# Kernel tuning notes

Hardware: AMD Instinct MI355X
Metric: run time of the kernel (lower is better)

Reference implementation:

```python
import jax, jax.numpy as jnp
import numpy as np

NEG_SLOPE = 0.2  # PyG GATConv default negative_slope


def _edges(B, C):
    # Fully-connected (no self) edges among the FIRST C nodes only (as in original
    # code, which ignores batch when building edge_index), plus self loops on all
    # B*C nodes (PyG GATConv add_self_loops=True default).
    N = B * C
    ij = np.array([(i, j) for i in range(C) for j in range(C) if i != j], dtype=np.int32)
    loops = np.arange(N, dtype=np.int32)
    src = jnp.concatenate([jnp.asarray(ij[:, 0]), jnp.asarray(loops)])
    dst = jnp.concatenate([jnp.asarray(ij[:, 1]), jnp.asarray(loops)])
    return src, dst, N


def _gat_conv(x2d, W, att_src, att_dst, bias, src, dst, N):
    h = x2d @ W                              # [N, Fout] linear projection (no bias)
    a_src = h @ att_src                      # [N] per-node src attention logit
    a_dst = h @ att_dst                      # [N] per-node dst attention logit
    e = jax.nn.leaky_relu(a_src[src] + a_dst[dst], NEG_SLOPE)   # [E] edge scores
    m = jax.ops.segment_max(e, dst, num_segments=N)             # segment softmax
    ex = jnp.exp(e - m[dst])
    denom = jax.ops.segment_sum(ex, dst, num_segments=N)
    alpha = ex / denom[dst]                                     # [E]
    out = jax.ops.segment_sum(alpha[:, None] * h[src], dst, num_segments=N)
    return out + bias


def setup_inputs() -> dict:
    key = jax.random.key(0)
    k1, k2, k3, k4 = jax.random.split(key, 4)
    B, C, Fin, Fout = 2048, 63, 250, 250
    x = jax.random.normal(k1, (B, 1, C, Fin), dtype=jnp.float32)
    W = jax.random.normal(k2, (Fin, Fout), dtype=jnp.float32) / np.sqrt(Fin).astype(np.float32)
    att_src = jax.random.normal(k3, (Fout,), dtype=jnp.float32) / np.sqrt(Fout).astype(np.float32)
    att_dst = jax.random.normal(k4, (Fout,), dtype=jnp.float32) / np.sqrt(Fout).astype(np.float32)
    bias = jnp.zeros((Fout,), dtype=jnp.float32)
    return {"x": x, "W": W, "att_src": att_src, "att_dst": att_dst, "bias": bias}


def reference(x, W, att_src, att_dst, bias):
    B, _, C, F = x.shape
    src, dst, N = _edges(B, C)
    out = _gat_conv(x.reshape(N, F), W, att_src, att_dst, bias, src, dst, N)
    return out.reshape(B, 1, C, -1)   # [B, 1, C, Fout]
```

## Files before the change

### kernel.cpp

```cpp
#include <hip/hip_runtime.h>
#include <hip/hip_bf16.h>

#define FIN 250
#define NROWS 129024
#define NT 8
#define NBLK 1008

typedef short short8 __attribute__((ext_vector_type(8)));
typedef float f32x4 __attribute__((ext_vector_type(4)));

__device__ __forceinline__ short f2bf(float f) {
    __bf16 b = (__bf16)f;
    return __builtin_bit_cast(short, b);
}

#define WAITV(n) asm volatile("s_waitcnt vmcnt(" #n ")" ::: "memory")
#define WAITL    asm volatile("s_waitcnt lgkmcnt(0)" ::: "memory")
#define SCHEDF   __builtin_amdgcn_sched_barrier(0)
#define HWBAR do { asm volatile("" ::: "memory"); __builtin_amdgcn_s_barrier(); \
                   asm volatile("" ::: "memory"); } while (0)

#define AFR0 0
#define AFR1 8192
#define OB   16384

__device__ __forceinline__ void load_tile(uint4 (&lb)[4], const float* __restrict__ x,
                                          const float* __restrict__ xlast,
                                          int tile, int wv, int lane) {
    #pragma unroll
    for (int rr = 0; rr < 4; ++rr) {
        int grow = tile * 16 + wv * 4 + rr;
        const char* g = (grow == NROWS - 1) ? (const char*)xlast
                                            : (const char*)x + (size_t)grow * 1000u;
        lb[rr] = *(const uint4*)(g + lane * 16);
    }
}

__global__ void __launch_bounds__(256)
wt_prep(const float* __restrict__ W, const float* __restrict__ x,
        unsigned* __restrict__ Wt, float* __restrict__ xlast) {
    int i = blockIdx.x * 256 + threadIdx.x;
    unsigned c  = (unsigned)i >> 7;
    unsigned kp = (unsigned)i & 127u;
    unsigned k0 = 2u * kp;
    unsigned lo = 0u, hi = 0u;
    if (c < FIN) {
        if (k0 < FIN)      lo = (unsigned)(unsigned short)f2bf(W[k0 * FIN + c]);
        if (k0 + 1u < FIN) hi = (unsigned)(unsigned short)f2bf(W[(k0 + 1u) * FIN + c]);
    }
    Wt[(c << 7) + kp] = lo | (hi << 16);
    if (blockIdx.x == 0) {
        int t = threadIdx.x;
        xlast[t] = (t < FIN) ? x[(size_t)(NROWS - 1) * FIN + t] : 0.f;
    }
}

__global__ void __launch_bounds__(256, 1)
gat_gemm(const float* __restrict__ x, const unsigned short* __restrict__ Wt,
         const float* __restrict__ xlast, const float* __restrict__ bias,
         float* __restrict__ out)
{
    __shared__ __align__(16) char lds[32768];

    const int tid  = threadIdx.x;
    const int lane = tid & 63;
    const int wv   = tid >> 6;
    const int m    = lane & 15;
    const int kg   = lane >> 4;

    short8 b[4][8];
    #pragma unroll
    for (int f = 0; f < 4; ++f)
        #pragma unroll
        for (int kk = 0; kk < 8; ++kk)
            b[f][kk] = *(const short8*)((const char*)Wt
                         + ((size_t)(wv * 64 + f * 16 + m) << 9) + kk * 64 + kg * 16);

    float bc[4];
    #pragma unroll
    for (int f = 0; f < 4; ++f) {
        int c = wv * 64 + f * 16 + m;
        bc[f] = (c < FIN) ? bias[c] : 0.f;
    }

    char* const ob = lds + OB;
    const int wkk   = lane >> 3;
    const int wkg   = (lane >> 1) & 3;
    const int whalf = lane & 1;
    const unsigned wroff = (unsigned)(wkk * 1024 + wkg * 256 + whalf * 8);

    WAITV(0); SCHEDF;

    const int bid = blockIdx.x;
    uint4 lbA[4], lbB[4];
    load_tile(lbA, x, xlast, bid,        wv, lane);
    load_tile(lbB, x, xlast, bid + NBLK, wv, lane);
    SCHEDF;

    #pragma unroll 1
    for (int i = 0; i < NT; ++i) {
        const int t = bid + i * NBLK;
        switch (i) {
            case 0:      WAITV(4);  break;
            case 1:      WAITV(12); break;
            case NT - 1: WAITV(16); break;
            default:     WAITV(20); break;
        }
        SCHEDF;

        {
            char* const afrD = lds + ((i & 1) ? AFR1 : AFR0);
            const uint4* lb = (i & 1) ? lbB : lbA;
            #pragma unroll
            for (int rr = 0; rr < 4; ++rr) {
                int row = wv * 4 + rr;
                float v0 = __builtin_bit_cast(float, lb[rr].x);
                float v1 = __builtin_bit_cast(float, lb[rr].y);
                float v2 = __builtin_bit_cast(float, lb[rr].z);
                float v3 = __builtin_bit_cast(float, lb[rr].w);
                unsigned lo = (unsigned)(unsigned short)f2bf(v0)
                            | ((unsigned)(unsigned short)f2bf(v1) << 16);
                unsigned hi = (unsigned)(unsigned short)f2bf(v2)
                            | ((unsigned)(unsigned short)f2bf(v3) << 16);
                *(uint2*)(afrD + wroff + (unsigned)(((row ^ wkk) * 16)))
                    = make_uint2(lo, hi);
            }
        }
        SCHEDF;
        if (i + 2 < NT) {
            if (i & 1) load_tile(lbB, x, xlast, t + 2 * NBLK, wv, lane);
            else       load_tile(lbA, x, xlast, t + 2 * NBLK, wv, lane);
        }
        SCHEDF;
        WAITL;
        HWBAR;

        const char* afrD = lds + ((i & 1) ? AFR1 : AFR0);
        f32x4 acc[4];
        #pragma unroll
        for (int f = 0; f < 4; ++f) acc[f] = (f32x4){bc[f], bc[f], bc[f], bc[f]};
        #pragma unroll
        for (int kk = 0; kk < 8; ++kk) {
            short8 af = *(const short8*)(afrD + kk * 1024 + kg * 256 + ((m ^ kk) * 16));
            #pragma unroll
            for (int f = 0; f < 4; ++f)
                acc[f] = __builtin_amdgcn_mfma_f32_16x16x32_bf16(af, b[f][kk], acc[f], 0, 0, 0);
        }

        #pragma unroll
        for (int f = 0; f < 4; ++f)
            #pragma unroll
            for (int j = 0; j < 4; ++j)
                *(float*)(ob + (kg * 4 + j) * 1024 + (unsigned)(wv * 64 + f * 16 + m) * 4)
                    = acc[f][j];
        WAITL;
        HWBAR;

        #pragma unroll
        for (int rr = 0; rr < 4; ++rr) {
            int row = wv * 4 + rr;
            float4 v = *(const float4*)(ob + row * 1024 + lane * 16);
            char* op = (char*)out + ((size_t)t * 16 + row) * 1000u;
            if (lane < 62)  *(float4*)(op + lane * 16) = v;
            if (lane == 62) *(float2*)(op + 992) = make_float2(v.x, v.y);
        }
    }
}

__global__ void __launch_bounds__(1024, 1)
gat_attn(const float* __restrict__ att_src, const float* __restrict__ att_dst,
         float* __restrict__ out)
{
    __shared__ float hs[63 * 252];
    __shared__ float asrc[64], adst[64];
    __shared__ float alpha[63 * 64];

    const int tid = threadIdx.x;

    for (int idx = tid; idx < 63 * FIN; idx += 1024) {
        int r = idx / FIN, f = idx - r * FIN;
        hs[r * 252 + f] = out[idx];
    }
    __syncthreads();

    {
        int r = tid >> 4, t = tid & 15;
        float s1 = 0.f, s2 = 0.f;
        if (r < 63) {
            for (int k = t; k < FIN; k += 16) {
                float h = hs[r * 252 + k];
                s1 += h * att_src[k];
                s2 += h * att_dst[k];
            }
        }
        #pragma unroll
        for (int o = 8; o >= 1; o >>= 1) {
            s1 += __shfl_xor(s1, o, 16);
            s2 += __shfl_xor(s2, o, 16);
        }
        if (r < 63 && t == 0) { asrc[r] = s1; adst[r] = s2; }
    }
    __syncthreads();

    {
        int d = tid >> 4, t = tid & 15;
        if (d < 63) {
            float ad = adst[d];
            float e_[4];
            float mx = -1e30f;
            #pragma unroll
            for (int q = 0; q < 4; ++q) {
                int sdx = t + q * 16;
                float e = -1e30f;
                if (sdx < 63) {
                    e = asrc[sdx] + ad;
                    e = e > 0.f ? e : 0.2f * e;
                }
                e_[q] = e;
                mx = fmaxf(mx, e);
            }
            #pragma unroll
            for (int o = 8; o >= 1; o >>= 1) mx = fmaxf(mx, __shfl_xor(mx, o, 16));
            float den = 0.f;
            #pragma unroll
            for (int q = 0; q < 4; ++q) {
                int sdx = t + q * 16;
                float ex = (sdx < 63) ? __expf(e_[q] - mx) : 0.f;
                e_[q] = ex;
                den += ex;
            }
            #pragma unroll
            for (int o = 8; o >= 1; o >>= 1) den += __shfl_xor(den, o, 16);
            float rd = 1.f / den;
            #pragma unroll
            for (int q = 0; q < 4; ++q) {
                int sdx = t + q * 16;
                if (sdx < 63) alpha[d * 64 + sdx] = e_[q] * rd;
            }
        }
    }
    __syncthreads();

    for (int idx = tid; idx < 63 * FIN; idx += 1024) {
        int d = idx / FIN, f = idx - d * FIN;
        float v = 0.f;
        for (int sdx = 0; sdx < 63; ++sdx)
            v += alpha[d * 64 + sdx] * hs[sdx * 252 + f];
        out[idx] = v;
    }
}

extern "C" void kernel_launch(void* const* d_in, const int* in_sizes, int n_in,
                              void* d_out, int out_size, void* d_ws, size_t ws_size,
                              hipStream_t stream) {
    (void)in_sizes; (void)n_in; (void)ws_size; (void)out_size;
    const float* x        = (const float*)d_in[0];
    const float* W        = (const float*)d_in[1];
    const float* att_src  = (const float*)d_in[2];
    const float* att_dst  = (const float*)d_in[3];
    const float* bias     = (const float*)d_in[4];
    float* out            = (float*)d_out;
    unsigned* Wt          = (unsigned*)d_ws;
    float* xlast          = (float*)((char*)d_ws + 131072);

    wt_prep<<<128, 256, 0, stream>>>(W, x, Wt, xlast);
    gat_gemm<<<NBLK, 256, 0, stream>>>(x, (const unsigned short*)Wt, xlast, bias, out);
    gat_attn<<<1, 1024, 0, stream>>>(att_src, att_dst, out);
}
```

Baseline: 93.50 us.

## Stage swizzled bf16 W in LDS and give each wave whole 16-row tiles

The block now copies the full bf16 W matrix, XOR-swizzled by wt_prep, into 160KB of LDS. Each wave then independently computes full 16x256 output tiles, reading B fragments from LDS instead of holding a 64-column slice in registers. This removes the per-tile block barriers and the LDS staging of outputs, since results go straight to global memory. The grid drops to 252 blocks with one wave per tile, and the next tile's load is overlapped between the two N-halves. The trade-offs are more LDS traffic for B, uncoalesced scalar output stores, and 16 uint4 load registers per lane.

Measured after the change: 106.4 us. 1.14x slower.

```diff
diff --git a/kernel.cpp b/kernel.cpp
--- a/kernel.cpp
+++ b/kernel.cpp
@@ -4,7 +4,8 @@
 #define FIN 250
 #define NROWS 129024
 #define NT 8
-#define NBLK 1008
+#define NBLK 252
+#define NWAVES 1008
 
 typedef short short8 __attribute__((ext_vector_type(8)));
 typedef float f32x4 __attribute__((ext_vector_type(4)));
@@ -17,22 +18,52 @@
 #define WAITV(n) asm volatile("s_waitcnt vmcnt(" #n ")" ::: "memory")
 #define WAITL    asm volatile("s_waitcnt lgkmcnt(0)" ::: "memory")
 #define SCHEDF   __builtin_amdgcn_sched_barrier(0)
-#define HWBAR do { asm volatile("" ::: "memory"); __builtin_amdgcn_s_barrier(); \
-                   asm volatile("" ::: "memory"); } while (0)
-
-#define AFR0 0
-#define AFR1 8192
-#define OB   16384
-
-__device__ __forceinline__ void load_tile(uint4 (&lb)[4], const float* __restrict__ x,
-                                          const float* __restrict__ xlast,
-                                          int tile, int wv, int lane) {
-    #pragma unroll
-    for (int rr = 0; rr < 4; ++rr) {
-        int grow = tile * 16 + wv * 4 + rr;
+
+#define AFR_BASE 131072
+
+__device__ __forceinline__ void load_tile16(uint4 (&lb)[16], const float* __restrict__ x,
+                                            const float* __restrict__ xlast,
+                                            int tile, int lane) {
+    #pragma unroll
+    for (int rr = 0; rr < 16; ++rr) {
+        int grow = tile * 16 + rr;
         const char* g = (grow == NROWS - 1) ? (const char*)xlast
                                             : (const char*)x + (size_t)grow * 1000u;
         lb[rr] = *(const uint4*)(g + lane * 16);
+    }
+}
+
+__device__ __forceinline__ void mfma_half(const char* afr, const char* wt,
+                                          float* __restrict__ out,
+                                          int tile, int half, int m, int kg,
+                                          unsigned bswz, const float (&bcol)[16]) {
+    f32x4 acc[8];
+    #pragma unroll
+    for (int nf = 0; nf < 8; ++nf) {
+        float b = bcol[half * 8 + nf];
+        acc[nf] = (f32x4){b, b, b, b};
+    }
+    const unsigned chbase = (unsigned)(half * 128) * 512u;
+    #pragma unroll
+    for (int kk = 0; kk < 8; ++kk) {
+        short8 af = *(const short8*)(afr + kk * 1024 + kg * 256 + ((m ^ kk) * 16));
+        #pragma unroll
+        for (int nf = 0; nf < 8; ++nf) {
+            unsigned off = chbase + (unsigned)(nf * 16 + m) * 512u
+                         + (((unsigned)(kk * 64 + kg * 16)) ^ bswz);
+            short8 bf = *(const short8*)(wt + off);
+            acc[nf] = __builtin_amdgcn_mfma_f32_16x16x32_bf16(af, bf, acc[nf], 0, 0, 0);
+        }
+    }
+    unsigned obase = ((unsigned)tile * 16 + (unsigned)kg * 4) * FIN
+                   + (unsigned)(half * 128 + m);
+    #pragma unroll
+    for (int nf = 0; nf < 8; ++nf) {
+        if (half == 0 || nf < 7 || m < 10) {
+            #pragma unroll
+            for (int j = 0; j < 4; ++j)
+                out[obase + (unsigned)(j * FIN) + (unsigned)(nf * 16)] = acc[nf][j];
+        }
     }
 }
 
@@ -40,15 +71,16 @@
 wt_prep(const float* __restrict__ W, const float* __restrict__ x,
         unsigned* __restrict__ Wt, float* __restrict__ xlast) {
     int i = blockIdx.x * 256 + threadIdx.x;
-    unsigned c  = (unsigned)i >> 7;
-    unsigned kp = (unsigned)i & 127u;
+    unsigned c  = (unsigned)i & 255u;
+    unsigned kp = (unsigned)i >> 8;
     unsigned k0 = 2u * kp;
     unsigned lo = 0u, hi = 0u;
     if (c < FIN) {
         if (k0 < FIN)      lo = (unsigned)(unsigned short)f2bf(W[k0 * FIN + c]);
         if (k0 + 1u < FIN) hi = (unsigned)(unsigned short)f2bf(W[(k0 + 1u) * FIN + c]);
     }
-    Wt[(c << 7) + kp] = lo | (hi << 16);
+    unsigned off = (c << 9) + ((4u * kp) ^ ((c & 7u) << 4));
+    *(unsigned*)((char*)Wt + off) = lo | (hi << 16);
     if (blockIdx.x == 0) {
         int t = threadIdx.x;
         xlast[t] = (t < FIN) ? x[(size_t)(NROWS - 1) * FIN + t] : 0.f;
@@ -56,11 +88,11 @@
 }
 
 __global__ void __launch_bounds__(256, 1)
-gat_gemm(const float* __restrict__ x, const unsigned short* __restrict__ Wt,
+gat_gemm(const float* __restrict__ x, const unsigned* __restrict__ Wt,
          const float* __restrict__ xlast, const float* __restrict__ bias,
          float* __restrict__ out)
 {
-    __shared__ __align__(16) char lds[32768];
+    __shared__ __align__(16) char lds[163840];
 
     const int tid  = threadIdx.x;
     const int lane = tid & 63;
@@ -68,22 +100,22 @@
     const int m    = lane & 15;
     const int kg   = lane >> 4;
 
-    short8 b[4][8];
-    #pragma unroll
-    for (int f = 0; f < 4; ++f)
-        #pragma unroll
-        for (int kk = 0; kk < 8; ++kk)
-            b[f][kk] = *(const short8*)((const char*)Wt
-                         + ((size_t)(wv * 64 + f * 16 + m) << 9) + kk * 64 + kg * 16);
-
-    float bc[4];
-    #pragma unroll
-    for (int f = 0; f < 4; ++f) {
-        int c = wv * 64 + f * 16 + m;
-        bc[f] = (c < FIN) ? bias[c] : 0.f;
-    }
-
-    char* const ob = lds + OB;
+    {
+        const uint4* s4 = (const uint4*)Wt;
+        uint4* d4 = (uint4*)lds;
+        for (int i = tid; i < 8192; i += 256) d4[i] = s4[i];
+    }
+    __syncthreads();
+
+    const unsigned bswz = ((unsigned)(m & 7)) << 4;
+    float bcol[16];
+    #pragma unroll
+    for (int nf = 0; nf < 16; ++nf) {
+        int c = nf * 16 + m;
+        bcol[nf] = (c < FIN) ? bias[c] : 0.f;
+    }
+
+    char* const afr = lds + AFR_BASE + wv * 8192;
     const int wkk   = lane >> 3;
     const int wkg   = (lane >> 1) & 3;
     const int whalf = lane & 1;
@@ -91,79 +123,36 @@
 
     WAITV(0); SCHEDF;
 
-    const int bid = blockIdx.x;
-    uint4 lbA[4], lbB[4];
-    load_tile(lbA, x, xlast, bid,        wv, lane);
-    load_tile(lbB, x, xlast, bid + NBLK, wv, lane);
-    SCHEDF;
+    const int w0 = blockIdx.x * 4 + wv;
+    uint4 lb[16];
+    load_tile16(lb, x, xlast, w0, lane);
 
     #pragma unroll 1
     for (int i = 0; i < NT; ++i) {
-        const int t = bid + i * NBLK;
-        switch (i) {
-            case 0:      WAITV(4);  break;
-            case 1:      WAITV(12); break;
-            case NT - 1: WAITV(16); break;
-            default:     WAITV(20); break;
-        }
-        SCHEDF;
-
-        {
-            char* const afrD = lds + ((i & 1) ? AFR1 : AFR0);
-            const uint4* lb = (i & 1) ? lbB : lbA;
-            #pragma unroll
-            for (int rr = 0; rr < 4; ++rr) {
-                int row = wv * 4 + rr;
-                float v0 = __builtin_bit_cast(float, lb[rr].x);
-                float v1 = __builtin_bit_cast(float, lb[rr].y);
-                float v2 = __builtin_bit_cast(float, lb[rr].z);
-                float v3 = __builtin_bit_cast(float, lb[rr].w);
-                unsigned lo = (unsigned)(unsigned short)f2bf(v0)
-                            | ((unsigned)(unsigned short)f2bf(v1) << 16);
-                unsigned hi = (unsigned)(unsigned short)f2bf(v2)
-                            | ((unsigned)(unsigned short)f2bf(v3) << 16);
-                *(uint2*)(afrD + wroff + (unsigned)(((row ^ wkk) * 16)))
-                    = make_uint2(lo, hi);
-            }
-        }
-        SCHEDF;
-        if (i + 2 < NT) {
-            if (i & 1) load_tile(lbB, x, xlast, t + 2 * NBLK, wv, lane);
-            else       load_tile(lbA, x, xlast, t + 2 * NBLK, wv, lane);
+        const int t = w0 + i * NWAVES;
+        if (i == 0) { WAITV(0); } else { WAITV(32); }
+        SCHEDF;
+
+        #pragma unroll
+        for (int rr = 0; rr < 16; ++rr) {
+            float v0 = __builtin_bit_cast(float, lb[rr].x);
+            float v1 = __builtin_bit_cast(float, lb[rr].y);
+            float v2 = __builtin_bit_cast(float, lb[rr].z);
+            float v3 = __builtin_bit_cast(float, lb[rr].w);
+            unsigned lo = (unsigned)(unsigned short)f2bf(v0)
+                        | ((unsigned)(unsigned short)f2bf(v1) << 16);
+            unsigned hi = (unsigned)(unsigned short)f2bf(v2)
+                        | ((unsigned)(unsigned short)f2bf(v3) << 16);
+            *(uint2*)(afr + wroff + (unsigned)(((rr ^ wkk) * 16))) = make_uint2(lo, hi);
         }
         SCHEDF;
         WAITL;
-        HWBAR;
-
-        const char* afrD = lds + ((i & 1) ? AFR1 : AFR0);
-        f32x4 acc[4];
-        #pragma unroll
-        for (int f = 0; f < 4; ++f) acc[f] = (f32x4){bc[f], bc[f], bc[f], bc[f]};
-        #pragma unroll
-        for (int kk = 0; kk < 8; ++kk) {
-            short8 af = *(const short8*)(afrD + kk * 1024 + kg * 256 + ((m ^ kk) * 16));
-            #pragma unroll
-            for (int f = 0; f < 4; ++f)
-                acc[f] = __builtin_amdgcn_mfma_f32_16x16x32_bf16(af, b[f][kk], acc[f], 0, 0, 0);
-        }
-
-        #pragma unroll
-        for (int f = 0; f < 4; ++f)
-            #pragma unroll
-            for (int j = 0; j < 4; ++j)
-                *(float*)(ob + (kg * 4 + j) * 1024 + (unsigned)(wv * 64 + f * 16 + m) * 4)
-                    = acc[f][j];
-        WAITL;
-        HWBAR;
-
-        #pragma unroll
-        for (int rr = 0; rr < 4; ++rr) {
-            int row = wv * 4 + rr;
-            float4 v = *(const float4*)(ob + row * 1024 + lane * 16);
-            char* op = (char*)out + ((size_t)t * 16 + row) * 1000u;
-            if (lane < 62)  *(float4*)(op + lane * 16) = v;
-            if (lane == 62) *(float2*)(op + 992) = make_float2(v.x, v.y);
-        }
+        SCHEDF;
+
+        mfma_half(afr, lds, out, t, 0, m, kg, bswz, bcol);
+        if (i + 1 < NT) load_tile16(lb, x, xlast, t + NWAVES, lane);
+        SCHEDF;
+        mfma_half(afr, lds, out, t, 1, m, kg, bswz, bcol);
     }
 }
 
@@ -264,6 +253,6 @@
     float* xlast          = (float*)((char*)d_ws + 131072);
 
     wt_prep<<<128, 256, 0, stream>>>(W, x, Wt, xlast);
-    gat_gemm<<<NBLK, 256, 0, stream>>>(x, (const unsigned short*)Wt, xlast, bias, out);
+    gat_gemm<<<NBLK, 256, 0, stream>>>(x, Wt, xlast, bias, out);
     gat_attn<<<1, 1024, 0, stream>>>(att_src, att_dst, out);
 }
```

## Make each wave load full tile and store output directly, removing block barriers

Applied to the files above, without the earlier changes.

Each wave now loads and converts all 16 input rows into its own private LDS region instead of sharing a block-wide staged tile, so both s_barrier calls disappear. The output is written straight from the MFMA accumulators with strided scalar stores, replacing the LDS staging pass that gave coalesced row writes. Prefetch drops from two tiles ahead to one. In exchange, every wave reads the same input rows, so global and L2 load traffic rises about fourfold, stores become narrow and scattered, and there is less latency hiding in what looks like a bandwidth-bound kernel.

Result: slower. 106.9 us (+14.4%).

```diff
diff --git a/kernel.cpp b/kernel.cpp
--- a/kernel.cpp
+++ b/kernel.cpp
@@ -17,19 +17,13 @@
 #define WAITV(n) asm volatile("s_waitcnt vmcnt(" #n ")" ::: "memory")
 #define WAITL    asm volatile("s_waitcnt lgkmcnt(0)" ::: "memory")
 #define SCHEDF   __builtin_amdgcn_sched_barrier(0)
-#define HWBAR do { asm volatile("" ::: "memory"); __builtin_amdgcn_s_barrier(); \
-                   asm volatile("" ::: "memory"); } while (0)
-
-#define AFR0 0
-#define AFR1 8192
-#define OB   16384
-
-__device__ __forceinline__ void load_tile(uint4 (&lb)[4], const float* __restrict__ x,
-                                          const float* __restrict__ xlast,
-                                          int tile, int wv, int lane) {
+
+__device__ __forceinline__ void load_tile16(uint4 (&lb)[16], const float* __restrict__ x,
+                                            const float* __restrict__ xlast,
+                                            int tile, int lane) {
     #pragma unroll
-    for (int rr = 0; rr < 4; ++rr) {
-        int grow = tile * 16 + wv * 4 + rr;
+    for (int rr = 0; rr < 16; ++rr) {
+        int grow = tile * 16 + rr;
         const char* g = (grow == NROWS - 1) ? (const char*)xlast
                                             : (const char*)x + (size_t)grow * 1000u;
         lb[rr] = *(const uint4*)(g + lane * 16);
@@ -83,7 +77,7 @@
         bc[f] = (c < FIN) ? bias[c] : 0.f;
     }
 
-    char* const ob = lds + OB;
+    char* const afr = lds + wv * 8192;
     const int wkk   = lane >> 3;
     const int wkg   = (lane >> 1) & 3;
     const int whalf = lane & 1;
@@ -92,77 +86,55 @@
     WAITV(0); SCHEDF;
 
     const int bid = blockIdx.x;
-    uint4 lbA[4], lbB[4];
-    load_tile(lbA, x, xlast, bid,        wv, lane);
-    load_tile(lbB, x, xlast, bid + NBLK, wv, lane);
+    uint4 lb[16];
+    load_tile16(lb, x, xlast, bid, lane);
     SCHEDF;
 
     #pragma unroll 1
     for (int i = 0; i < NT; ++i) {
         const int t = bid + i * NBLK;
-        switch (i) {
-            case 0:      WAITV(4);  break;
-            case 1:      WAITV(12); break;
-            case NT - 1: WAITV(16); break;
-            default:     WAITV(20); break;
-        }
-        SCHEDF;
-
-        {
-            char* const afrD = lds + ((i & 1) ? AFR1 : AFR0);
-            const uint4* lb = (i & 1) ? lbB : lbA;
-            #pragma unroll
-            for (int rr = 0; rr < 4; ++rr) {
-                int row = wv * 4 + rr;
-                float v0 = __builtin_bit_cast(float, lb[rr].x);
-                float v1 = __builtin_bit_cast(float, lb[rr].y);
-                float v2 = __builtin_bit_cast(float, lb[rr].z);
-                float v3 = __builtin_bit_cast(float, lb[rr].w);
-                unsigned lo = (unsigned)(unsigned short)f2bf(v0)
-                            | ((unsigned)(unsigned short)f2bf(v1) << 16);
-                unsigned hi = (unsigned)(unsigned short)f2bf(v2)
-                            | ((unsigned)(unsigned short)f2bf(v3) << 16);
-                *(uint2*)(afrD + wroff + (unsigned)(((row ^ wkk) * 16)))
-                    = make_uint2(lo, hi);
-            }
-        }
-        SCHEDF;
-        if (i + 2 < NT) {
-            if (i & 1) load_tile(lbB, x, xlast, t + 2 * NBLK, wv, lane);
-            else       load_tile(lbA, x, xlast, t + 2 * NBLK, wv, lane);
-        }
+        if (i == 0) { WAITV(0); } else { WAITV(16); }
+        SCHEDF;
+
+        #pragma unroll
+        for (int rr = 0; rr < 16; ++rr) {
+            float v0 = __builtin_bit_cast(float, lb[rr].x);
+            float v1 = __builtin_bit_cast(float, lb[rr].y);
+            float v2 = __builtin_bit_cast(float, lb[rr].z);
+            float v3 = __builtin_bit_cast(float, lb[rr].w);
+            unsigned lo = (unsigned)(unsigned short)f2bf(v0)
+                        | ((unsigned)(unsigned short)f2bf(v1) << 16);
+            unsigned hi = (unsigned)(unsigned short)f2bf(v2)
+                        | ((unsigned)(unsigned short)f2bf(v3) << 16);
+            *(uint2*)(afr + wroff + (unsigned)(((rr ^ wkk) * 16))) = make_uint2(lo, hi);
+        }
+        SCHEDF;
+        if (i + 1 < NT) load_tile16(lb, x, xlast, t + NBLK, lane);
         SCHEDF;
         WAITL;
-        HWBAR;
-
-        const char* afrD = lds + ((i & 1) ? AFR1 : AFR0);
+        SCHEDF;
+
         f32x4 acc[4];
         #pragma unroll
         for (int f = 0; f < 4; ++f) acc[f] = (f32x4){bc[f], bc[f], bc[f], bc[f]};
         #pragma unroll
         for (int kk = 0; kk < 8; ++kk) {
-            short8 af = *(const short8*)(afrD + kk * 1024 + kg * 256 + ((m ^ kk) * 16));
+            short8 af = *(const short8*)(afr + kk * 1024 + kg * 256 + ((m ^ kk) * 16));
             #pragma unroll
             for (int f = 0; f < 4; ++f)
                 acc[f] = __builtin_amdgcn_mfma_f32_16x16x32_bf16(af, b[f][kk], acc[f], 0, 0, 0);
         }
 
-        #pragma unroll
-        for (int f = 0; f < 4; ++f)
-            #pragma unroll
-            for (int j = 0; j < 4; ++j)
-                *(float*)(ob + (kg * 4 + j) * 1024 + (unsigned)(wv * 64 + f * 16 + m) * 4)
-                    = acc[f][j];
-        WAITL;
-        HWBAR;
-
-        #pragma unroll
-        for (int rr = 0; rr < 4; ++rr) {
-            int row = wv * 4 + rr;
-            float4 v = *(const float4*)(ob + row * 1024 + lane * 16);
-            char* op = (char*)out + ((size_t)t * 16 + row) * 1000u;
-            if (lane < 62)  *(float4*)(op + lane * 16) = v;
-            if (lane == 62) *(float2*)(op + 992) = make_float2(v.x, v.y);
+        unsigned obase = ((unsigned)t * 16 + (unsigned)kg * 4) * FIN
+                       + (unsigned)(wv * 64 + m);
+        #pragma unroll
+        for (int f = 0; f < 4; ++f) {
+            bool ok = (wv < 3) || (f < 3) || (m < 10);
+            if (ok) {
+                #pragma unroll
+                for (int j = 0; j < 4; ++j)
+                    out[obase + (unsigned)(f * 16) + (unsigned)(j * FIN)] = acc[f][j];
+            }
         }
     }
 }
```
